# Kernel optimization log

Hardware: AMD Instinct MI355X
Metric: run time of the kernel (lower is better)

Reference implementation:

```python
import jax, jax.numpy as jnp
import numpy as np

B, IN_CAPS, IN_DIM = 64, 512, 128
NUM_CAPS, DIM_CAPS, NUM_ROUTING = 32, 32, 3


def squash(x, axis=-1):
    sn = jnp.sum(x * x, axis=axis, keepdims=True)
    return (sn / (1.0 + sn)) * x / (jnp.sqrt(sn) + 1e-8)


def setup_inputs() -> dict:
    key = jax.random.key(0)
    k1, k2, k3 = jax.random.split(key, 3)
    input_tensor = jax.random.normal(k1, (B, IN_CAPS, IN_DIM), dtype=jnp.float32)
    W = 0.001 * jax.random.normal(k2, (NUM_CAPS, IN_DIM, DIM_CAPS), dtype=jnp.float32)
    b0 = jax.random.uniform(k3, (B, NUM_CAPS, IN_CAPS, 1), dtype=jnp.float32)
    return {"input_tensor": input_tensor, "W": W, "b0": b0}


def reference(input_tensor, W, b0):
    # u_hat: (B, num_caps, in_caps, dim_caps)
    u_hat = jnp.einsum('bid,ndc->bnic', input_tensor, W)
    temp_u_hat = jax.lax.stop_gradient(u_hat)
    b = b0
    for _ in range(NUM_ROUTING - 1):
        c = jax.nn.softmax(b, axis=1)            # (B, num_caps, in_caps, 1)
        s = jnp.sum(c * temp_u_hat, axis=2)      # (B, num_caps, dim_caps)
        v = squash(s)
        uv = jnp.einsum('bnic,bnc->bni', temp_u_hat, v)[..., None]
        b = b + uv
    c = jax.nn.softmax(b, axis=1)
    s = jnp.sum(c * u_hat, axis=2)
    return squash(s)                             # (B, num_caps, dim_caps)
```

## Files before the change

### kernel.cpp

```cpp
#include <hip/hip_runtime.h>
#include <math.h>

#define Bsz 64
#define IC  512
#define KD  128
#define NC  32
#define DC  32
#define CHUNK 64
#define NCH   8
#define NBLK  512
#define NTHR  256

#define CSTR 36
#define BSTR 68

#define CXP_SZ (Bsz * NCH * NC * KD)
#define WV_SZ  (Bsz * NC * KD)

__device__ __forceinline__ int xaddr(int i, int kq) {
    return i * KD + ((((kq) + (i >> 2)) & 31) << 2);
}

__global__ __launch_bounds__(NTHR, 2)
void kA(const float* __restrict__ bb_in, const float* __restrict__ x_g,
        const float* __restrict__ wv_g, float* __restrict__ bb_out,
        float* __restrict__ cxp, int do_uv, int write_bb)
{
    __shared__ float x_s[CHUNK * KD];
    __shared__ float bb_s[NC * BSTR];
    __shared__ float scr[KD * CSTR];

    const int t = threadIdx.x, blk = blockIdx.x;
    const int b = blk & 63, ch = blk >> 6, i0g = ch * CHUNK;

    for (int rep = 0; rep < 8; ++rep) {
        int v = t + rep * NTHR;
        int i = v >> 5, kq = v & 31;
        *(float4*)(x_s + xaddr(i, kq)) =
            *(const float4*)(x_g + ((size_t)(b * IC + i0g + i)) * KD + (kq << 2));
    }
    for (int rep = 0; rep < 2; ++rep) {
        int v = t + rep * NTHR;
        int n = v >> 4, i4 = v & 15;
        *(float4*)(bb_s + n * BSTR + (i4 << 2)) =
            *(const float4*)(bb_in + ((size_t)(b * NC + n)) * IC + i0g + (i4 << 2));
    }
    if (do_uv) {
        for (int rep = 0; rep < 4; ++rep) {
            const int n = t & 31;
            const int k4 = (t >> 5) + (rep << 3);
            float4 v4 = *(const float4*)(wv_g + ((size_t)(b * NC) + n) * KD + (k4 << 2));
            scr[(k4 * 4 + 0) * CSTR + n] = v4.x;
            scr[(k4 * 4 + 1) * CSTR + n] = v4.y;
            scr[(k4 * 4 + 2) * CSTR + n] = v4.z;
            scr[(k4 * 4 + 3) * CSTR + n] = v4.w;
        }
    }
    __syncthreads();

    if (do_uv) {
        const int tt = t & 127;
        const int tn = tt & 7, ti = tt >> 3;
        const int n0 = tn << 2, i0 = ti << 2;
        const int kq0 = (t >> 7) << 4;
        float4 a0 = {0,0,0,0}, a1 = {0,0,0,0}, a2 = {0,0,0,0}, a3 = {0,0,0,0};
        for (int kq = kq0; kq < kq0 + 16; ++kq) {
            const float4 xr0 = *(const float4*)(x_s + xaddr(i0 + 0, kq));
            const float4 xr1 = *(const float4*)(x_s + xaddr(i0 + 1, kq));
            const float4 xr2 = *(const float4*)(x_s + xaddr(i0 + 2, kq));
            const float4 xr3 = *(const float4*)(x_s + xaddr(i0 + 3, kq));
            const float4 w0 = *(const float4*)(scr + (kq * 4 + 0) * CSTR + n0);
            const float4 w1 = *(const float4*)(scr + (kq * 4 + 1) * CSTR + n0);
            const float4 w2 = *(const float4*)(scr + (kq * 4 + 2) * CSTR + n0);
            const float4 w3 = *(const float4*)(scr + (kq * 4 + 3) * CSTR + n0);
            a0.x += xr0.x*w0.x + xr0.y*w1.x + xr0.z*w2.x + xr0.w*w3.x;
            a0.y += xr0.x*w0.y + xr0.y*w1.y + xr0.z*w2.y + xr0.w*w3.y;
            a0.z += xr0.x*w0.z + xr0.y*w1.z + xr0.z*w2.z + xr0.w*w3.z;
            a0.w += xr0.x*w0.w + xr0.y*w1.w + xr0.z*w2.w + xr0.w*w3.w;
            a1.x += xr1.x*w0.x + xr1.y*w1.x + xr1.z*w2.x + xr1.w*w3.x;
            a1.y += xr1.x*w0.y + xr1.y*w1.y + xr1.z*w2.y + xr1.w*w3.y;
            a1.z += xr1.x*w0.z + xr1.y*w1.z + xr1.z*w2.z + xr1.w*w3.z;
            a1.w += xr1.x*w0.w + xr1.y*w1.w + xr1.z*w2.w + xr1.w*w3.w;
            a2.x += xr2.x*w0.x + xr2.y*w1.x + xr2.z*w2.x + xr2.w*w3.x;
            a2.y += xr2.x*w0.y + xr2.y*w1.y + xr2.z*w2.y + xr2.w*w3.y;
            a2.z += xr2.x*w0.z + xr2.y*w1.z + xr2.z*w2.z + xr2.w*w3.z;
            a2.w += xr2.x*w0.w + xr2.y*w1.w + xr2.z*w2.w + xr2.w*w3.w;
            a3.x += xr3.x*w0.x + xr3.y*w1.x + xr3.z*w2.x + xr3.w*w3.x;
            a3.y += xr3.x*w0.y + xr3.y*w1.y + xr3.z*w2.y + xr3.w*w3.y;
            a3.z += xr3.x*w0.z + xr3.y*w1.z + xr3.z*w2.z + xr3.w*w3.z;
            a3.w += xr3.x*w0.w + xr3.y*w1.w + xr3.z*w2.w + xr3.w*w3.w;
        }
        atomicAdd(&bb_s[(n0+0)*BSTR + i0+0], a0.x);
        atomicAdd(&bb_s[(n0+1)*BSTR + i0+0], a0.y);
        atomicAdd(&bb_s[(n0+2)*BSTR + i0+0], a0.z);
        atomicAdd(&bb_s[(n0+3)*BSTR + i0+0], a0.w);
        atomicAdd(&bb_s[(n0+0)*BSTR + i0+1], a1.x);
        atomicAdd(&bb_s[(n0+1)*BSTR + i0+1], a1.y);
        atomicAdd(&bb_s[(n0+2)*BSTR + i0+1], a1.z);
        atomicAdd(&bb_s[(n0+3)*BSTR + i0+1], a1.w);
        atomicAdd(&bb_s[(n0+0)*BSTR + i0+2], a2.x);
        atomicAdd(&bb_s[(n0+1)*BSTR + i0+2], a2.y);
        atomicAdd(&bb_s[(n0+2)*BSTR + i0+2], a2.z);
        atomicAdd(&bb_s[(n0+3)*BSTR + i0+2], a2.w);
        atomicAdd(&bb_s[(n0+0)*BSTR + i0+3], a3.x);
        atomicAdd(&bb_s[(n0+1)*BSTR + i0+3], a3.y);
        atomicAdd(&bb_s[(n0+2)*BSTR + i0+3], a3.z);
        atomicAdd(&bb_s[(n0+3)*BSTR + i0+3], a3.w);
        __syncthreads();
        if (write_bb) {
            for (int rep = 0; rep < 2; ++rep) {
                int v = t + rep * NTHR;
                int n = v >> 4, i4 = v & 15;
                *(float4*)(bb_out + ((size_t)(b * NC + n)) * IC + i0g + (i4 << 2)) =
                    *(const float4*)(bb_s + n * BSTR + (i4 << 2));
            }
        }
    }

    if (t < CHUNK) {
        const int ii = t;
        float m = -1e30f;
        #pragma unroll
        for (int n = 0; n < NC; ++n) m = fmaxf(m, bb_s[n * BSTR + ii]);
        float e[NC]; float sum = 0.f;
        #pragma unroll
        for (int n = 0; n < NC; ++n) { float ev = __expf(bb_s[n * BSTR + ii] - m); e[n] = ev; sum += ev; }
        const float inv = 1.f / sum;
        float* crow = scr + ii * CSTR;
        #pragma unroll
        for (int n = 0; n < NC; ++n) crow[n] = e[n] * inv;
    }
    __syncthreads();

    {
        const int tn = t & 7, tk = t >> 3;
        const int n0 = tn << 2;
        float4 acc0 = {0,0,0,0}, acc1 = {0,0,0,0}, acc2 = {0,0,0,0}, acc3 = {0,0,0,0};
        for (int ii = 0; ii < CHUNK; ++ii) {
            const float4 c4 = *(const float4*)(scr + ii * CSTR + n0);
            const float4 x4 = *(const float4*)(x_s + xaddr(ii, tk));
            acc0.x += c4.x*x4.x; acc0.y += c4.x*x4.y; acc0.z += c4.x*x4.z; acc0.w += c4.x*x4.w;
            acc1.x += c4.y*x4.x; acc1.y += c4.y*x4.y; acc1.z += c4.y*x4.z; acc1.w += c4.y*x4.w;
            acc2.x += c4.z*x4.x; acc2.y += c4.z*x4.y; acc2.z += c4.z*x4.z; acc2.w += c4.z*x4.w;
            acc3.x += c4.w*x4.x; acc3.y += c4.w*x4.y; acc3.z += c4.w*x4.z; acc3.w += c4.w*x4.w;
        }
        float* base = cxp + ((size_t)(b * NCH + ch)) * NC * KD + (tk << 2);
        *(float4*)(base + (size_t)(n0 + 0) * KD) = acc0;
        *(float4*)(base + (size_t)(n0 + 1) * KD) = acc1;
        *(float4*)(base + (size_t)(n0 + 2) * KD) = acc2;
        *(float4*)(base + (size_t)(n0 + 3) * KD) = acc3;
    }
}

__global__ __launch_bounds__(NTHR, 2)
void kB(const float* __restrict__ cxp, const float* __restrict__ W_g,
        float* __restrict__ wv_g, float* __restrict__ out_g, int final_)
{
    __shared__ float cxs[4 * KD];
    __shared__ float vb[4 * DC];

    const int t = threadIdx.x, blk = blockIdx.x;
    const int b = blk & 63, ng = blk >> 6;
    const int w = t >> 6, l = t & 63;
    const int n = (ng << 2) + w;

    {
        float c0 = 0.f, c1 = 0.f;
        const float* p = cxp + ((size_t)b * NCH * NC + n) * KD;
        #pragma unroll
        for (int c2 = 0; c2 < NCH; ++c2) {
            c0 += p[(size_t)c2 * NC * KD + l];
            c1 += p[(size_t)c2 * NC * KD + l + 64];
        }
        cxs[w * KD + l] = c0; cxs[w * KD + l + 64] = c1;
    }
    __syncthreads();

    const int dgrp = l & 7, d0 = dgrp << 2, kg = l >> 3;
    const float* Wn = W_g + (size_t)n * KD * DC;
    const float* cxw = cxs + w * KD;
    float4 acc = {0,0,0,0};
    #pragma unroll
    for (int j = 0; j < 16; ++j) {
        const int k = (j << 3) + kg;
        const float4 w4 = *(const float4*)(Wn + (size_t)k * DC + d0);
        const float cv = cxw[k];
        acc.x += cv * w4.x; acc.y += cv * w4.y; acc.z += cv * w4.z; acc.w += cv * w4.w;
    }
    #pragma unroll
    for (int off = 8; off < 64; off <<= 1) {
        acc.x += __shfl_xor(acc.x, off, 64);
        acc.y += __shfl_xor(acc.y, off, 64);
        acc.z += __shfl_xor(acc.z, off, 64);
        acc.w += __shfl_xor(acc.w, off, 64);
    }
    float ss = acc.x*acc.x + acc.y*acc.y + acc.z*acc.z + acc.w*acc.w;
    #pragma unroll
    for (int off = 1; off < 8; off <<= 1) ss += __shfl_xor(ss, off, 64);
    const float scale = ss / ((1.f + ss) * (sqrtf(ss) + 1e-8f));
    float4 v4; v4.x = acc.x*scale; v4.y = acc.y*scale; v4.z = acc.z*scale; v4.w = acc.w*scale;

    if (final_) {
        if (kg == 0) *(float4*)(out_g + ((size_t)(b * NC) + n) * DC + d0) = v4;
    } else {
        float* vbw = vb + w * DC;
        if (kg == 0) *(float4*)(vbw + d0) = v4;
        __syncthreads();
        float wv0 = 0.f, wv1 = 0.f;
        #pragma unroll
        for (int j = 0; j < 8; ++j) {
            const float4 vv = *(const float4*)(vbw + (j << 2));
            const float4 wa = *(const float4*)(Wn + (size_t)l * DC + (j << 2));
            const float4 wb = *(const float4*)(Wn + (size_t)(l + 64) * DC + (j << 2));
            wv0 += wa.x*vv.x + wa.y*vv.y + wa.z*vv.z + wa.w*vv.w;
            wv1 += wb.x*vv.x + wb.y*vv.y + wb.z*vv.z + wb.w*vv.w;
        }
        float* wrow = wv_g + ((size_t)(b * NC) + n) * KD;
        wrow[l] = wv0; wrow[l + 64] = wv1;
    }
}

extern "C" void kernel_launch(void* const* d_in, const int* in_sizes, int n_in,
                              void* d_out, int out_size, void* d_ws, size_t ws_size,
                              hipStream_t stream) {
    const float* x  = (const float*)d_in[0];
    const float* W  = (const float*)d_in[1];
    const float* b0 = (const float*)d_in[2];
    float* out = (float*)d_out;

    float* cxp   = (float*)d_ws;
    float* wv    = cxp + CXP_SZ;
    float* bb_ws = wv + WV_SZ;

    kA<<<NBLK, NTHR, 0, stream>>>(b0, x, nullptr, nullptr, cxp, 0, 0);
    kB<<<NBLK, NTHR, 0, stream>>>(cxp, W, wv, nullptr, 0);
    kA<<<NBLK, NTHR, 0, stream>>>(b0, x, wv, bb_ws, cxp, 1, 1);
    kB<<<NBLK, NTHR, 0, stream>>>(cxp, W, wv, nullptr, 0);
    kA<<<NBLK, NTHR, 0, stream>>>(bb_ws, x, wv, nullptr, cxp, 1, 0);
    kB<<<NBLK, NTHR, 0, stream>>>(cxp, W, nullptr, out, 1);
}
```

Before: 144.7 us.

## Stage W in shared memory in kB, remap block indices, drop LDS atomics

Result: faster. 128.0 us (-11.5%).

```diff
diff --git a/kernel.cpp b/kernel.cpp
--- a/kernel.cpp
+++ b/kernel.cpp
@@ -13,6 +13,7 @@
 
 #define CSTR 36
 #define BSTR 68
+#define WSTR 33
 
 #define CXP_SZ (Bsz * NCH * NC * KD)
 #define WV_SZ  (Bsz * NC * KD)
@@ -21,7 +22,7 @@
     return i * KD + ((((kq) + (i >> 2)) & 31) << 2);
 }
 
-__global__ __launch_bounds__(NTHR, 2)
+__global__ __launch_bounds__(NTHR)
 void kA(const float* __restrict__ bb_in, const float* __restrict__ x_g,
         const float* __restrict__ wv_g, float* __restrict__ bb_out,
         float* __restrict__ cxp, int do_uv, int write_bb)
@@ -31,7 +32,7 @@
     __shared__ float scr[KD * CSTR];
 
     const int t = threadIdx.x, blk = blockIdx.x;
-    const int b = blk & 63, ch = blk >> 6, i0g = ch * CHUNK;
+    const int b = blk >> 3, ch = blk & 7, i0g = ch * CHUNK;
 
     for (int rep = 0; rep < 8; ++rep) {
         int v = t + rep * NTHR;
@@ -59,53 +60,45 @@
     __syncthreads();
 
     if (do_uv) {
-        const int tt = t & 127;
-        const int tn = tt & 7, ti = tt >> 3;
-        const int n0 = tn << 2, i0 = ti << 2;
-        const int kq0 = (t >> 7) << 4;
-        float4 a0 = {0,0,0,0}, a1 = {0,0,0,0}, a2 = {0,0,0,0}, a3 = {0,0,0,0};
-        for (int kq = kq0; kq < kq0 + 16; ++kq) {
-            const float4 xr0 = *(const float4*)(x_s + xaddr(i0 + 0, kq));
-            const float4 xr1 = *(const float4*)(x_s + xaddr(i0 + 1, kq));
-            const float4 xr2 = *(const float4*)(x_s + xaddr(i0 + 2, kq));
-            const float4 xr3 = *(const float4*)(x_s + xaddr(i0 + 3, kq));
-            const float4 w0 = *(const float4*)(scr + (kq * 4 + 0) * CSTR + n0);
-            const float4 w1 = *(const float4*)(scr + (kq * 4 + 1) * CSTR + n0);
-            const float4 w2 = *(const float4*)(scr + (kq * 4 + 2) * CSTR + n0);
-            const float4 w3 = *(const float4*)(scr + (kq * 4 + 3) * CSTR + n0);
-            a0.x += xr0.x*w0.x + xr0.y*w1.x + xr0.z*w2.x + xr0.w*w3.x;
-            a0.y += xr0.x*w0.y + xr0.y*w1.y + xr0.z*w2.y + xr0.w*w3.y;
-            a0.z += xr0.x*w0.z + xr0.y*w1.z + xr0.z*w2.z + xr0.w*w3.z;
-            a0.w += xr0.x*w0.w + xr0.y*w1.w + xr0.z*w2.w + xr0.w*w3.w;
-            a1.x += xr1.x*w0.x + xr1.y*w1.x + xr1.z*w2.x + xr1.w*w3.x;
-            a1.y += xr1.x*w0.y + xr1.y*w1.y + xr1.z*w2.y + xr1.w*w3.y;
-            a1.z += xr1.x*w0.z + xr1.y*w1.z + xr1.z*w2.z + xr1.w*w3.z;
-            a1.w += xr1.x*w0.w + xr1.y*w1.w + xr1.z*w2.w + xr1.w*w3.w;
-            a2.x += xr2.x*w0.x + xr2.y*w1.x + xr2.z*w2.x + xr2.w*w3.x;
-            a2.y += xr2.x*w0.y + xr2.y*w1.y + xr2.z*w2.y + xr2.w*w3.y;
-            a2.z += xr2.x*w0.z + xr2.y*w1.z + xr2.z*w2.z + xr2.w*w3.z;
-            a2.w += xr2.x*w0.w + xr2.y*w1.w + xr2.z*w2.w + xr2.w*w3.w;
-            a3.x += xr3.x*w0.x + xr3.y*w1.x + xr3.z*w2.x + xr3.w*w3.x;
-            a3.y += xr3.x*w0.y + xr3.y*w1.y + xr3.z*w2.y + xr3.w*w3.y;
-            a3.z += xr3.x*w0.z + xr3.y*w1.z + xr3.z*w2.z + xr3.w*w3.z;
-            a3.w += xr3.x*w0.w + xr3.y*w1.w + xr3.z*w2.w + xr3.w*w3.w;
-        }
-        atomicAdd(&bb_s[(n0+0)*BSTR + i0+0], a0.x);
-        atomicAdd(&bb_s[(n0+1)*BSTR + i0+0], a0.y);
-        atomicAdd(&bb_s[(n0+2)*BSTR + i0+0], a0.z);
-        atomicAdd(&bb_s[(n0+3)*BSTR + i0+0], a0.w);
-        atomicAdd(&bb_s[(n0+0)*BSTR + i0+1], a1.x);
-        atomicAdd(&bb_s[(n0+1)*BSTR + i0+1], a1.y);
-        atomicAdd(&bb_s[(n0+2)*BSTR + i0+1], a1.z);
-        atomicAdd(&bb_s[(n0+3)*BSTR + i0+1], a1.w);
-        atomicAdd(&bb_s[(n0+0)*BSTR + i0+2], a2.x);
-        atomicAdd(&bb_s[(n0+1)*BSTR + i0+2], a2.y);
-        atomicAdd(&bb_s[(n0+2)*BSTR + i0+2], a2.z);
-        atomicAdd(&bb_s[(n0+3)*BSTR + i0+2], a2.w);
-        atomicAdd(&bb_s[(n0+0)*BSTR + i0+3], a3.x);
-        atomicAdd(&bb_s[(n0+1)*BSTR + i0+3], a3.y);
-        atomicAdd(&bb_s[(n0+2)*BSTR + i0+3], a3.z);
-        atomicAdd(&bb_s[(n0+3)*BSTR + i0+3], a3.w);
+        if (t < 128) {
+            const int tn = t & 7, ti = t >> 3;
+            const int n0 = tn << 2, i0 = ti << 2;
+            float4 a0 = {0,0,0,0}, a1 = {0,0,0,0}, a2 = {0,0,0,0}, a3 = {0,0,0,0};
+            for (int kq = 0; kq < 32; ++kq) {
+                const float4 xr0 = *(const float4*)(x_s + xaddr(i0 + 0, kq));
+                const float4 xr1 = *(const float4*)(x_s + xaddr(i0 + 1, kq));
+                const float4 xr2 = *(const float4*)(x_s + xaddr(i0 + 2, kq));
+                const float4 xr3 = *(const float4*)(x_s + xaddr(i0 + 3, kq));
+                const float4 w0 = *(const float4*)(scr + (kq * 4 + 0) * CSTR + n0);
+                const float4 w1 = *(const float4*)(scr + (kq * 4 + 1) * CSTR + n0);
+                const float4 w2 = *(const float4*)(scr + (kq * 4 + 2) * CSTR + n0);
+                const float4 w3 = *(const float4*)(scr + (kq * 4 + 3) * CSTR + n0);
+                a0.x += xr0.x*w0.x + xr0.y*w1.x + xr0.z*w2.x + xr0.w*w3.x;
+                a0.y += xr0.x*w0.y + xr0.y*w1.y + xr0.z*w2.y + xr0.w*w3.y;
+                a0.z += xr0.x*w0.z + xr0.y*w1.z + xr0.z*w2.z + xr0.w*w3.z;
+                a0.w += xr0.x*w0.w + xr0.y*w1.w + xr0.z*w2.w + xr0.w*w3.w;
+                a1.x += xr1.x*w0.x + xr1.y*w1.x + xr1.z*w2.x + xr1.w*w3.x;
+                a1.y += xr1.x*w0.y + xr1.y*w1.y + xr1.z*w2.y + xr1.w*w3.y;
+                a1.z += xr1.x*w0.z + xr1.y*w1.z + xr1.z*w2.z + xr1.w*w3.z;
+                a1.w += xr1.x*w0.w + xr1.y*w1.w + xr1.z*w2.w + xr1.w*w3.w;
+                a2.x += xr2.x*w0.x + xr2.y*w1.x + xr2.z*w2.x + xr2.w*w3.x;
+                a2.y += xr2.x*w0.y + xr2.y*w1.y + xr2.z*w2.y + xr2.w*w3.y;
+                a2.z += xr2.x*w0.z + xr2.y*w1.z + xr2.z*w2.z + xr2.w*w3.z;
+                a2.w += xr2.x*w0.w + xr2.y*w1.w + xr2.z*w2.w + xr2.w*w3.w;
+                a3.x += xr3.x*w0.x + xr3.y*w1.x + xr3.z*w2.x + xr3.w*w3.x;
+                a3.y += xr3.x*w0.y + xr3.y*w1.y + xr3.z*w2.y + xr3.w*w3.y;
+                a3.z += xr3.x*w0.z + xr3.y*w1.z + xr3.z*w2.z + xr3.w*w3.z;
+                a3.w += xr3.x*w0.w + xr3.y*w1.w + xr3.z*w2.w + xr3.w*w3.w;
+            }
+            bb_s[(n0+0)*BSTR + i0+0] += a0.x; bb_s[(n0+1)*BSTR + i0+0] += a0.y;
+            bb_s[(n0+2)*BSTR + i0+0] += a0.z; bb_s[(n0+3)*BSTR + i0+0] += a0.w;
+            bb_s[(n0+0)*BSTR + i0+1] += a1.x; bb_s[(n0+1)*BSTR + i0+1] += a1.y;
+            bb_s[(n0+2)*BSTR + i0+1] += a1.z; bb_s[(n0+3)*BSTR + i0+1] += a1.w;
+            bb_s[(n0+0)*BSTR + i0+2] += a2.x; bb_s[(n0+1)*BSTR + i0+2] += a2.y;
+            bb_s[(n0+2)*BSTR + i0+2] += a2.z; bb_s[(n0+3)*BSTR + i0+2] += a2.w;
+            bb_s[(n0+0)*BSTR + i0+3] += a3.x; bb_s[(n0+1)*BSTR + i0+3] += a3.y;
+            bb_s[(n0+2)*BSTR + i0+3] += a3.z; bb_s[(n0+3)*BSTR + i0+3] += a3.w;
+        }
         __syncthreads();
         if (write_bb) {
             for (int rep = 0; rep < 2; ++rep) {
@@ -152,21 +145,29 @@
     }
 }
 
-__global__ __launch_bounds__(NTHR, 2)
+__global__ __launch_bounds__(NTHR)
 void kB(const float* __restrict__ cxp, const float* __restrict__ W_g,
         float* __restrict__ wv_g, float* __restrict__ out_g, int final_)
 {
+    __shared__ float w_s[KD * WSTR];
     __shared__ float cxs[4 * KD];
     __shared__ float vb[4 * DC];
 
     const int t = threadIdx.x, blk = blockIdx.x;
-    const int b = blk & 63, ng = blk >> 6;
+    const int pb_n = blk & 31, pb_b0 = (blk >> 5) * 4;
     const int w = t >> 6, l = t & 63;
-    const int n = (ng << 2) + w;
-
+    const int b = pb_b0 + w;
+
+    for (int rep = 0; rep < 4; ++rep) {
+        int v = t + rep * NTHR;
+        int k = v >> 3, d0 = (v & 7) << 2;
+        float4 w4 = *(const float4*)(W_g + (size_t)pb_n * KD * DC + ((size_t)v << 2));
+        float* dst = w_s + k * WSTR + d0;
+        dst[0] = w4.x; dst[1] = w4.y; dst[2] = w4.z; dst[3] = w4.w;
+    }
     {
         float c0 = 0.f, c1 = 0.f;
-        const float* p = cxp + ((size_t)b * NCH * NC + n) * KD;
+        const float* p = cxp + ((size_t)b * NCH * NC + pb_n) * KD;
         #pragma unroll
         for (int c2 = 0; c2 < NCH; ++c2) {
             c0 += p[(size_t)c2 * NC * KD + l];
@@ -177,15 +178,14 @@
     __syncthreads();
 
     const int dgrp = l & 7, d0 = dgrp << 2, kg = l >> 3;
-    const float* Wn = W_g + (size_t)n * KD * DC;
     const float* cxw = cxs + w * KD;
     float4 acc = {0,0,0,0};
     #pragma unroll
     for (int j = 0; j < 16; ++j) {
         const int k = (j << 3) + kg;
-        const float4 w4 = *(const float4*)(Wn + (size_t)k * DC + d0);
+        const float* wr = w_s + k * WSTR + d0;
         const float cv = cxw[k];
-        acc.x += cv * w4.x; acc.y += cv * w4.y; acc.z += cv * w4.z; acc.w += cv * w4.w;
+        acc.x += cv * wr[0]; acc.y += cv * wr[1]; acc.z += cv * wr[2]; acc.w += cv * wr[3];
     }
     #pragma unroll
     for (int off = 8; off < 64; off <<= 1) {
@@ -201,7 +201,7 @@
     float4 v4; v4.x = acc.x*scale; v4.y = acc.y*scale; v4.z = acc.z*scale; v4.w = acc.w*scale;
 
     if (final_) {
-        if (kg == 0) *(float4*)(out_g + ((size_t)(b * NC) + n) * DC + d0) = v4;
+        if (kg == 0) *(float4*)(out_g + ((size_t)(b * NC) + pb_n) * DC + d0) = v4;
     } else {
         float* vbw = vb + w * DC;
         if (kg == 0) *(float4*)(vbw + d0) = v4;
@@ -210,12 +210,12 @@
         #pragma unroll
         for (int j = 0; j < 8; ++j) {
             const float4 vv = *(const float4*)(vbw + (j << 2));
-            const float4 wa = *(const float4*)(Wn + (size_t)l * DC + (j << 2));
-            const float4 wb = *(const float4*)(Wn + (size_t)(l + 64) * DC + (j << 2));
-            wv0 += wa.x*vv.x + wa.y*vv.y + wa.z*vv.z + wa.w*vv.w;
-            wv1 += wb.x*vv.x + wb.y*vv.y + wb.z*vv.z + wb.w*vv.w;
-        }
-        float* wrow = wv_g + ((size_t)(b * NC) + n) * KD;
+            const float* wa = w_s + l * WSTR + (j << 2);
+            const float* wb = w_s + (l + 64) * WSTR + (j << 2);
+            wv0 += wa[0]*vv.x + wa[1]*vv.y + wa[2]*vv.z + wa[3]*vv.w;
+            wv1 += wb[0]*vv.x + wb[1]*vv.y + wb[2]*vv.z + wb[3]*vv.w;
+        }
+        float* wrow = wv_g + ((size_t)(b * NC) + pb_n) * KD;
         wrow[l] = wv0; wrow[l + 64] = wv1;
     }
 }
```
